# Kernel optimization log

Hardware: AMD Instinct MI355X
Metric: run time of the kernel (lower is better)

The kernel has to match this reference:

```python
import jax, jax.numpy as jnp
import numpy as np

# ---- static configuration (mirrors module init kwargs) ----
RADIUS = 8.0
MAX_NEIGHBORS = 32          # max_num_neighbors_threshold
MAX_REP = (2, 2, 0)         # static: rep = min(ceil(radius*inv_min_dist), threshold) = 2 for a1,a2; pbc[2]=False -> 0
B, N_ATOMS = 32, 128
CELL_EDGE = 4.0


def _unit_cells():
    # torch.cartesian_prod over arange(-rep, rep+1) per dim; pbc z disabled -> single 0
    ax = [np.arange(-r, r + 1, dtype=np.float32) for r in MAX_REP]
    g = np.stack(np.meshgrid(*ax, indexing='ij'), axis=-1).reshape(-1, 3)
    return jnp.asarray(g)  # [C, 3], C = 5*5*1 = 25


def setup_inputs() -> dict:
    key = jax.random.key(0)
    k1, k2 = jax.random.split(key)
    # near-cubic cells ~4A with small perturbation (keeps rep clamped at threshold=2)
    cell = (CELL_EDGE * jnp.eye(3, dtype=jnp.float32)[None] +
            0.05 * jax.random.normal(k2, (B, 3, 3), dtype=jnp.float32))
    # atoms at fractional coords in [0,1): pos = frac @ cell
    frac = jax.random.uniform(k1, (B, N_ATOMS, 3), dtype=jnp.float32)
    pos = jnp.einsum('bnf,bfk->bnk', frac, cell)
    return {'pos': pos, 'cell': cell}


def reference(pos, cell):
    """PBC radius-graph construction (gen_edges_from_batch), padded form.

    Candidate edges live on a fixed grid [B, i, j, c]: i = index1 (center atom),
    j = index2 (neighbor), c = periodic image. Returns:
      edge_dist       [B,N,N,C] f32  distance (0 where edge invalid)
      edge_cell_type  [B,N,N,C] i32  linearized cell-offset id (0 where invalid)
      edge_mask       [B,N,N,C] bool edge survives radius + self + kNN truncation
      num_neighbors_image [B]   i32  per-image edge counts (clamped), as in torch
    """
    u = _unit_cells()                         # [C,3]
    C = u.shape[0]
    # pbc offsets: offset_c = u_c @ cell_b  (matches cell_offsets.bmm(cell))
    off = jnp.einsum('ci,bik->bck', u, cell)  # [B,C,3]

    # distance vectors: pos[index2] - pos[index1] + offset (get_pbc_distances convention)
    dvec = (pos[:, None, :, None, :] - pos[:, :, None, None, :]
            + off[:, None, None, :, :])       # [B,N,N,C,3]
    d2 = jnp.sum(dvec * dvec, axis=-1)        # [B,N,N,C]

    within = (d2 <= RADIUS * RADIUS) & (d2 > 1e-4)

    # --- sort-based neighbor truncation per center atom i (get_max_neighbors_mask) ---
    num_atoms = B * N_ATOMS
    rows = jnp.where(within, d2, jnp.inf).reshape(num_atoms, N_ATOMS * C)
    order = jnp.argsort(rows, axis=1)         # stable: ties keep (j,c) order as torch
    ranks = jnp.argsort(order, axis=1)        # inverse permutation = rank of each cand
    keep = (ranks < MAX_NEIGHBORS).reshape(B, N_ATOMS, N_ATOMS, C) & within

    # per-image clamped neighbor counts (segment_csr of clamped segment_coo)
    num_nb = jnp.sum(within, axis=(2, 3)).astype(jnp.int32)          # [B,N]
    num_neighbors_image = jnp.sum(jnp.minimum(num_nb, MAX_NEIGHBORS), axis=1)

    safe_d2 = jnp.where(keep, d2, 1.0)
    edge_dist = jnp.where(keep, jnp.sqrt(safe_d2), 0.0)

    # linearized cell type: (offsets + max_rep) . [nr1*nr2, nr1, 1] with nr = 2*rep+1
    nr = np.array([2 * r + 1 for r in MAX_REP])
    mults = jnp.asarray([nr[1] * nr[2], nr[1], 1], dtype=jnp.int32)  # matches torch code
    ct = jnp.sum((u.astype(jnp.int32) + jnp.asarray(MAX_REP, jnp.int32)) * mults, axis=-1)  # [C]
    edge_cell_type = jnp.where(keep, ct[None, None, None, :], 0).astype(jnp.int32)

    return edge_dist, edge_cell_type, keep, num_neighbors_image
```

## Files before the change

### kernel.cpp

```cpp
#include <hip/hip_runtime.h>
#include <math.h>
#include <stdint.h>

#define NATOMS   128
#define NCELLS   25
#define NCAND    (NATOMS * NCELLS)
#define MAXNB    32
#define R2       64.0f
#define BLK      256
#define KEYCAP   192
#define DCUT     6.25f

__device__ __forceinline__ float d2_exact(float4 p, float4 ctr, float4 o) {
    float dx = __fadd_rn(__fsub_rn(p.x, ctr.x), o.x);
    float dy = __fadd_rn(__fsub_rn(p.y, ctr.y), o.y);
    float dz = __fadd_rn(__fsub_rn(p.z, ctr.z), o.z);
    return __fadd_rn(__fadd_rn(__fmul_rn(dx,dx), __fmul_rn(dy,dy)),
                     __fmul_rn(dz,dz));
}

__global__ __launch_bounds__(BLK) void graph_kernel(
    const float* __restrict__ pos, const float* __restrict__ cell,
    float* __restrict__ out_dist, float* __restrict__ out_ctype,
    float* __restrict__ out_mask, float* __restrict__ ws_counts)
{
    __shared__ float4 s_pos4[NATOMS];
    __shared__ float4 s_off4[NCELLS];
    __shared__ float  s_ct[NCELLS];
    __shared__ float  s_d2[NCAND];
    __shared__ unsigned long long s_keys[KEYCAP];
    __shared__ unsigned s_hist[256];
    __shared__ unsigned s_wtot[4];
    __shared__ int s_wred[4];
    __shared__ unsigned s_cnt, s_cnt2;
    __shared__ int s_tot, s_binsel, s_need;
    __shared__ unsigned long long s_K;

    const int bi   = blockIdx.x;
    const int b    = bi >> 7;
    const int i    = bi & 127;
    const int tid  = threadIdx.x;
    const int lane = tid & 63;
    const int w    = tid >> 6;

    if (tid < NATOMS) {
        const float* p = pos + (b * NATOMS + tid) * 3;
        s_pos4[tid] = make_float4(p[0], p[1], p[2], 0.0f);
    }
    if (tid >= 160 && tid < 160 + NCELLS) {
        int c = tid - 160;
        float ux = (float)(c / 5 - 2);
        float uy = (float)(c % 5 - 2);
        float ox = __fadd_rn(__fmul_rn(ux, cell[b*9+0]), __fmul_rn(uy, cell[b*9+3]));
        float oy = __fadd_rn(__fmul_rn(ux, cell[b*9+1]), __fmul_rn(uy, cell[b*9+4]));
        float oz = __fadd_rn(__fmul_rn(ux, cell[b*9+2]), __fmul_rn(uy, cell[b*9+5]));
        s_off4[c] = make_float4(ox, oy, oz, 0.0f);
        s_ct[c] = (float)(5 * (c / 5) + 5 * (c % 5));
    }
    if (tid == 0) { s_cnt = 0; s_cnt2 = 0; s_binsel = -1; s_need = 0; s_K = ~0ULL; }
    __syncthreads();

    const float4 ctr = s_pos4[i];

    int local = 0;
    for (int g = tid; g < NCAND; g += BLK) {
        int c = g >> 7;
        int j = g & 127;
        float d2 = d2_exact(s_pos4[j], ctr, s_off4[c]);
        bool within = (d2 <= R2) && (d2 > 1e-4f);
        int f = j * NCELLS + c;
        s_d2[f] = within ? d2 : __builtin_inff();
        local += within;
        bool sel = within && (d2 < DCUT);
        unsigned long long mb = __ballot(sel);
        if (mb) {
            unsigned cnt = (unsigned)__popcll(mb);
            unsigned base = 0;
            if (lane == 0) base = atomicAdd(&s_cnt, cnt);
            base = __shfl(base, 0);
            if (sel) {
                unsigned p = base + (unsigned)__popcll(mb & ((1ULL << lane) - 1ULL));
                if (p < KEYCAP)
                    s_keys[p] = ((unsigned long long)__float_as_uint(d2) << 32)
                                | (unsigned)f;
            }
        }
    }
    for (int o = 32; o; o >>= 1) local += __shfl_down(local, o);
    if (lane == 0) s_wred[w] = local;
    __syncthreads();
    if (tid == 0) {
        int tot = s_wred[0] + s_wred[1] + s_wred[2] + s_wred[3];
        s_tot = tot;
        ws_counts[bi] = (float)(tot < MAXNB ? tot : MAXNB);
    }
    __syncthreads();

    if (s_tot > MAXNB) {
        const unsigned m = s_cnt;
        if (m >= MAXNB && m <= KEYCAP) {
            for (unsigned p = tid; p < m; p += BLK) {
                unsigned long long kp = s_keys[p];
                int r = 0;
                for (unsigned q = 0; q < m; q++) r += (s_keys[q] < kp);
                if (r == MAXNB - 1) s_K = kp;
            }
        } else {
            s_hist[tid] = 0u;
            __syncthreads();
            for (int v = tid; v < NCAND / 4; v += BLK) {
                float4 dq = ((const float4*)s_d2)[v];
                #pragma unroll
                for (int e = 0; e < 4; e++) {
                    float d2 = (&dq.x)[e];
                    if (d2 < 64.5f) {
                        int bin = (int)(d2 * 4.0f);
                        if (bin > 255) bin = 255;
                        atomicAdd(&s_hist[bin], 1u);
                    }
                }
            }
            __syncthreads();
            unsigned h = s_hist[tid];
            int v = (int)h;
            #pragma unroll
            for (int off = 1; off < 64; off <<= 1) {
                int u = __shfl_up(v, off, 64);
                if (lane >= off) v += u;
            }
            if (lane == 63) s_wtot[w] = (unsigned)v;
            __syncthreads();
            unsigned pre = 0;
            for (int ww = 0; ww < w; ww++) pre += s_wtot[ww];
            unsigned ci = (unsigned)v + pre, ce = ci - h;
            if (h > 0 && ce < MAXNB && ci >= MAXNB) {
                s_binsel = tid;
                s_need   = MAXNB - (int)ce;
            }
            __syncthreads();
            const int binsel = s_binsel, need = s_need;
            for (int f = tid; f < NCAND; f += BLK) {
                float d2 = s_d2[f];
                if (d2 < 64.5f) {
                    int bin = (int)(d2 * 4.0f);
                    if (bin > 255) bin = 255;
                    if (bin == binsel) {
                        unsigned idx = atomicAdd(&s_cnt2, 1u);
                        if (idx < KEYCAP)
                            s_keys[idx] =
                                ((unsigned long long)__float_as_uint(d2) << 32)
                                | (unsigned)f;
                    }
                }
            }
            __syncthreads();
            const int m2 = (int)s_cnt2;
            if (m2 <= KEYCAP) {
                for (int p = tid; p < m2; p += BLK) {
                    unsigned long long kp = s_keys[p];
                    int r = 0;
                    for (int q = 0; q < m2; q++) r += (s_keys[q] < kp);
                    if (r == need - 1) s_K = kp;
                }
            } else {
                for (int f = tid; f < NCAND; f += BLK) {
                    float d2 = s_d2[f];
                    if (d2 >= 64.5f) continue;
                    int bin = (int)(d2 * 4.0f);
                    if (bin > 255) bin = 255;
                    if (bin != binsel) continue;
                    unsigned long long kf =
                        ((unsigned long long)__float_as_uint(d2) << 32)
                        | (unsigned)f;
                    int r = 0;
                    for (int q = 0; q < NCAND; q++) {
                        float dq = s_d2[q];
                        if (dq >= 64.5f) continue;
                        int bq = (int)(dq * 4.0f);
                        if (bq > 255) bq = 255;
                        if (bq != binsel) continue;
                        unsigned long long kq =
                            ((unsigned long long)__float_as_uint(dq) << 32)
                            | (unsigned)q;
                        r += (kq < kf);
                    }
                    if (r == need - 1) s_K = kf;
                }
            }
        }
    }
    __syncthreads();
    const unsigned long long K = s_K;

    const long long base = (long long)bi * NCAND;
    float4* o0 = (float4*)(out_dist  + base);
    float4* o1 = (float4*)(out_ctype + base);
    float4* o2 = (float4*)(out_mask  + base);
    for (int v = tid; v < NCAND / 4; v += BLK) {
        float4 dq = ((const float4*)s_d2)[v];
        int f0 = v * 4;
        int c = f0 % NCELLS;
        float4 r0, r1, r2;
        #pragma unroll
        for (int e = 0; e < 4; e++) {
            float d2 = (&dq.x)[e];
            bool within = (d2 <= R2);
            unsigned long long key =
                ((unsigned long long)__float_as_uint(d2) << 32)
                | (unsigned)(f0 + e);
            bool keep = within && (key <= K);
            (&r0.x)[e] = keep ? sqrtf(d2) : 0.0f;
            (&r1.x)[e] = keep ? s_ct[c] : 0.0f;
            (&r2.x)[e] = keep ? 1.0f : 0.0f;
            c++; if (c == NCELLS) c = 0;
        }
        o0[v] = r0; o1[v] = r1; o2[v] = r2;
    }
}

__global__ __launch_bounds__(64) void reduce_counts(
    const float* __restrict__ ws_counts, float* __restrict__ out_nb)
{
    int b = blockIdx.x;
    int t = threadIdx.x;
    float v = ws_counts[b * NATOMS + t] + ws_counts[b * NATOMS + 64 + t];
    for (int o = 32; o; o >>= 1) v += __shfl_down(v, o);
    if (t == 0) out_nb[b] = v;
}

extern "C" void kernel_launch(void* const* d_in, const int* in_sizes, int n_in,
                              void* d_out, int out_size, void* d_ws, size_t ws_size,
                              hipStream_t stream) {
    const float* pos  = (const float*)d_in[0];
    const float* cell = (const float*)d_in[1];
    float* out = (float*)d_out;
    const long long E = 32LL * NATOMS * NATOMS * NCELLS;
    float* out_dist  = out;
    float* out_ct    = out + E;
    float* out_mask  = out + 2 * E;
    float* out_nb    = out + 3 * E;
    float* ws = (float*)d_ws;

    hipLaunchKernelGGL(graph_kernel, dim3(32 * NATOMS), dim3(BLK), 0, stream,
                       pos, cell, out_dist, out_ct, out_mask, ws);
    hipLaunchKernelGGL(reduce_counts, dim3(32), dim3(64), 0, stream,
                       ws, out_nb);
}
```

Before: 165.0 us.

## Write zero output groups early and defer only near-candidate groups

The candidate loop now runs over groups of four in storage order. Any group with no candidate under the distance cut has its zero outputs written straight away, during the distance pass. Groups that contain close candidates are recorded in a shared todo list. On the fast path, only those groups are revisited after the threshold key is found. This overlaps most of the output stores with the compute and selection phases. It adds shared atomics, a ballot per element, and a correctness dependence on the todo-cap check. If the cap or any fast-path condition fails, the kernel falls back to the full rewrite path.

```diff
diff --git a/kernel.cpp b/kernel.cpp
--- a/kernel.cpp
+++ b/kernel.cpp
@@ -5,10 +5,12 @@
 #define NATOMS   128
 #define NCELLS   25
 #define NCAND    (NATOMS * NCELLS)
+#define NGRP     (NCAND / 4)
 #define MAXNB    32
 #define R2       64.0f
 #define BLK      256
 #define KEYCAP   192
+#define TODOCAP  256
 #define DCUT     6.25f
 
 __device__ __forceinline__ float d2_exact(float4 p, float4 ctr, float4 o) {
@@ -29,10 +31,11 @@
     __shared__ float  s_ct[NCELLS];
     __shared__ float  s_d2[NCAND];
     __shared__ unsigned long long s_keys[KEYCAP];
+    __shared__ unsigned short s_todo[TODOCAP];
     __shared__ unsigned s_hist[256];
     __shared__ unsigned s_wtot[4];
     __shared__ int s_wred[4];
-    __shared__ unsigned s_cnt, s_cnt2;
+    __shared__ unsigned s_cnt, s_cnt2, s_ntodo;
     __shared__ int s_tot, s_binsel, s_need;
     __shared__ unsigned long long s_K;
 
@@ -57,37 +60,66 @@
         s_off4[c] = make_float4(ox, oy, oz, 0.0f);
         s_ct[c] = (float)(5 * (c / 5) + 5 * (c % 5));
     }
-    if (tid == 0) { s_cnt = 0; s_cnt2 = 0; s_binsel = -1; s_need = 0; s_K = ~0ULL; }
+    if (tid == 0) {
+        s_cnt = 0; s_cnt2 = 0; s_ntodo = 0;
+        s_binsel = -1; s_need = 0; s_K = ~0ULL;
+    }
     __syncthreads();
 
     const float4 ctr = s_pos4[i];
-
-    int local = 0;
-    for (int g = tid; g < NCAND; g += BLK) {
-        int c = g >> 7;
-        int j = g & 127;
-        float d2 = d2_exact(s_pos4[j], ctr, s_off4[c]);
-        bool within = (d2 <= R2) && (d2 > 1e-4f);
-        int f = j * NCELLS + c;
-        s_d2[f] = within ? d2 : __builtin_inff();
-        local += within;
-        bool sel = within && (d2 < DCUT);
-        unsigned long long mb = __ballot(sel);
-        if (mb) {
-            unsigned cnt = (unsigned)__popcll(mb);
-            unsigned base = 0;
-            if (lane == 0) base = atomicAdd(&s_cnt, cnt);
-            base = __shfl(base, 0);
-            if (sel) {
-                unsigned p = base + (unsigned)__popcll(mb & ((1ULL << lane) - 1ULL));
-                if (p < KEYCAP)
-                    s_keys[p] = ((unsigned long long)__float_as_uint(d2) << 32)
-                                | (unsigned)f;
-            }
-        }
-    }
-    for (int o = 32; o; o >>= 1) local += __shfl_down(local, o);
-    if (lane == 0) s_wred[w] = local;
+    const long long base = (long long)bi * NGRP;
+    float4* o0 = (float4*)out_dist  + base;
+    float4* o1 = (float4*)out_ctype + base;
+    float4* o2 = (float4*)out_mask  + base;
+    const float4 z4 = make_float4(0.f, 0.f, 0.f, 0.f);
+
+    int nwithin = 0;
+    #pragma unroll 1
+    for (int k = 0; k < 4; k++) {
+        int g = tid + k * BLK;
+        if (g >= NGRP) continue;
+        int f0 = g * 4;
+        int j = f0 / 25;
+        int c = f0 - j * 25;
+        float d2e[4];
+        bool cl[4];
+        bool anyclose = false;
+        #pragma unroll
+        for (int e = 0; e < 4; e++) {
+            float d2 = d2_exact(s_pos4[j], ctr, s_off4[c]);
+            bool within = (d2 <= R2) && (d2 > 1e-4f);
+            d2e[e] = within ? d2 : __builtin_inff();
+            nwithin += within;
+            cl[e] = within && (d2 < DCUT);
+            anyclose |= cl[e];
+            c++; if (c == 25) { c = 0; j++; }
+        }
+        ((float4*)s_d2)[g] = make_float4(d2e[0], d2e[1], d2e[2], d2e[3]);
+        #pragma unroll
+        for (int e = 0; e < 4; e++) {
+            unsigned long long mb = __ballot(cl[e]);
+            if (mb) {
+                unsigned cnt = (unsigned)__popcll(mb);
+                unsigned kb = 0;
+                if (lane == 0) kb = atomicAdd(&s_cnt, cnt);
+                kb = __shfl(kb, 0);
+                if (cl[e]) {
+                    unsigned p = kb + (unsigned)__popcll(mb & ((1ULL << lane) - 1ULL));
+                    if (p < KEYCAP)
+                        s_keys[p] = ((unsigned long long)__float_as_uint(d2e[e]) << 32)
+                                    | (unsigned)(f0 + e);
+                }
+            }
+        }
+        if (anyclose) {
+            unsigned u = atomicAdd(&s_ntodo, 1u);
+            if (u < TODOCAP) s_todo[u] = (unsigned short)g;
+        } else {
+            o0[g] = z4; o1[g] = z4; o2[g] = z4;
+        }
+    }
+    for (int o = 32; o; o >>= 1) nwithin += __shfl_down(nwithin, o);
+    if (lane == 0) s_wred[w] = nwithin;
     __syncthreads();
     if (tid == 0) {
         int tot = s_wred[0] + s_wred[1] + s_wred[2] + s_wred[3];
@@ -96,19 +128,46 @@
     }
     __syncthreads();
 
-    if (s_tot > MAXNB) {
-        const unsigned m = s_cnt;
-        if (m >= MAXNB && m <= KEYCAP) {
-            for (unsigned p = tid; p < m; p += BLK) {
-                unsigned long long kp = s_keys[p];
-                int r = 0;
-                for (unsigned q = 0; q < m; q++) r += (s_keys[q] < kp);
-                if (r == MAXNB - 1) s_K = kp;
-            }
-        } else {
+    const unsigned m = s_cnt;
+    const bool fast = (s_tot > MAXNB) && (m >= MAXNB) && (m <= KEYCAP)
+                      && (s_ntodo <= TODOCAP);
+
+    if (fast) {
+        for (unsigned p = tid; p < m; p += BLK) {
+            unsigned long long kp = s_keys[p];
+            int r = 0;
+            for (unsigned q = 0; q < m; q++) r += (s_keys[q] < kp);
+            if (r == MAXNB - 1) s_K = kp;
+        }
+        __syncthreads();
+        const unsigned long long K = s_K;
+        const int nt = (int)s_ntodo;
+        for (int u = tid; u < nt; u += BLK) {
+            int g = s_todo[u];
+            int f0 = g * 4;
+            float4 dq = ((const float4*)s_d2)[g];
+            int c = f0 % NCELLS;
+            float4 r0, r1, r2;
+            #pragma unroll
+            for (int e = 0; e < 4; e++) {
+                float d2 = (&dq.x)[e];
+                bool within = (d2 <= R2);
+                unsigned long long key =
+                    ((unsigned long long)__float_as_uint(d2) << 32)
+                    | (unsigned)(f0 + e);
+                bool keep = within && (key <= K);
+                (&r0.x)[e] = keep ? sqrtf(d2) : 0.0f;
+                (&r1.x)[e] = keep ? s_ct[c] : 0.0f;
+                (&r2.x)[e] = keep ? 1.0f : 0.0f;
+                c++; if (c == NCELLS) c = 0;
+            }
+            o0[g] = r0; o1[g] = r1; o2[g] = r2;
+        }
+    } else {
+        if (s_tot > MAXNB) {
             s_hist[tid] = 0u;
             __syncthreads();
-            for (int v = tid; v < NCAND / 4; v += BLK) {
+            for (int v = tid; v < NGRP; v += BLK) {
                 float4 dq = ((const float4*)s_d2)[v];
                 #pragma unroll
                 for (int e = 0; e < 4; e++) {
@@ -188,33 +247,28 @@
                 }
             }
         }
-    }
-    __syncthreads();
-    const unsigned long long K = s_K;
-
-    const long long base = (long long)bi * NCAND;
-    float4* o0 = (float4*)(out_dist  + base);
-    float4* o1 = (float4*)(out_ctype + base);
-    float4* o2 = (float4*)(out_mask  + base);
-    for (int v = tid; v < NCAND / 4; v += BLK) {
-        float4 dq = ((const float4*)s_d2)[v];
-        int f0 = v * 4;
-        int c = f0 % NCELLS;
-        float4 r0, r1, r2;
-        #pragma unroll
-        for (int e = 0; e < 4; e++) {
-            float d2 = (&dq.x)[e];
-            bool within = (d2 <= R2);
-            unsigned long long key =
-                ((unsigned long long)__float_as_uint(d2) << 32)
-                | (unsigned)(f0 + e);
-            bool keep = within && (key <= K);
-            (&r0.x)[e] = keep ? sqrtf(d2) : 0.0f;
-            (&r1.x)[e] = keep ? s_ct[c] : 0.0f;
-            (&r2.x)[e] = keep ? 1.0f : 0.0f;
-            c++; if (c == NCELLS) c = 0;
-        }
-        o0[v] = r0; o1[v] = r1; o2[v] = r2;
+        __syncthreads();
+        const unsigned long long K = s_K;
+        for (int v = tid; v < NGRP; v += BLK) {
+            float4 dq = ((const float4*)s_d2)[v];
+            int f0 = v * 4;
+            int c = f0 % NCELLS;
+            float4 r0, r1, r2;
+            #pragma unroll
+            for (int e = 0; e < 4; e++) {
+                float d2 = (&dq.x)[e];
+                bool within = (d2 <= R2);
+                unsigned long long key =
+                    ((unsigned long long)__float_as_uint(d2) << 32)
+                    | (unsigned)(f0 + e);
+                bool keep = within && (key <= K);
+                (&r0.x)[e] = keep ? sqrtf(d2) : 0.0f;
+                (&r1.x)[e] = keep ? s_ct[c] : 0.0f;
+                (&r2.x)[e] = keep ? 1.0f : 0.0f;
+                c++; if (c == NCELLS) c = 0;
+            }
+            o0[v] = r0; o1[v] = r1; o2[v] = r2;
+        }
     }
 }
 
```

New measurement: 191.3 us. 1.16x slower.

## Split threshold selection into a wave-per-atom kernel ahead of the streaming write kernel

Applied to the files above, without the earlier changes.

A new select kernel has one wavefront per center atom compute distances, count neighbours and find the 32nd-smallest key with a wave-local ballot compaction and rank search, storing the threshold to workspace. The write kernel then recomputes distances on the fly and streams the three outputs without staging distances in shared memory or synchronising for selection, except for a histogram fallback path. The count reduction is folded into the write kernel, so there are still two launches. The cost is computing distances twice and an extra round trip through workspace, in exchange for a lean, bandwidth-bound write pass.

```diff
diff --git a/kernel.cpp b/kernel.cpp
--- a/kernel.cpp
+++ b/kernel.cpp
@@ -10,6 +10,8 @@
 #define BLK      256
 #define KEYCAP   192
 #define DCUT     6.25f
+#define ALLPASS  ((((unsigned long long)0x7F800000u) << 32) | 0xFFFFFFFFull)
+#define FALLBK   (~0ULL)
 
 __device__ __forceinline__ float d2_exact(float4 p, float4 ctr, float4 o) {
     float dx = __fadd_rn(__fsub_rn(p.x, ctr.x), o.x);
@@ -19,10 +21,96 @@
                      __fmul_rn(dz,dz));
 }
 
-__global__ __launch_bounds__(BLK) void graph_kernel(
+__global__ __launch_bounds__(BLK) void select_kernel(
     const float* __restrict__ pos, const float* __restrict__ cell,
+    unsigned long long* __restrict__ ws_K, float* __restrict__ ws_counts)
+{
+    __shared__ float4 s_pos4[NATOMS];
+    __shared__ float4 s_off4[NCELLS];
+    __shared__ unsigned long long s_wkeys[4][KEYCAP];
+
+    const int blk  = blockIdx.x;
+    const int b    = blk >> 5;
+    const int tid  = threadIdx.x;
+    const int lane = tid & 63;
+    const int wave = tid >> 6;
+    const int bi   = (blk << 2) + wave;
+    const int i    = bi & 127;
+
+    if (tid < NATOMS) {
+        const float* p = pos + (b * NATOMS + tid) * 3;
+        s_pos4[tid] = make_float4(p[0], p[1], p[2], 0.0f);
+    }
+    if (tid >= 160 && tid < 160 + NCELLS) {
+        int c = tid - 160;
+        float ux = (float)(c / 5 - 2);
+        float uy = (float)(c % 5 - 2);
+        float ox = __fadd_rn(__fmul_rn(ux, cell[b*9+0]), __fmul_rn(uy, cell[b*9+3]));
+        float oy = __fadd_rn(__fmul_rn(ux, cell[b*9+1]), __fmul_rn(uy, cell[b*9+4]));
+        float oz = __fadd_rn(__fmul_rn(ux, cell[b*9+2]), __fmul_rn(uy, cell[b*9+5]));
+        s_off4[c] = make_float4(ox, oy, oz, 0.0f);
+    }
+    __syncthreads();
+
+    const float4 ctr = s_pos4[i];
+    const unsigned long long lmlt = (1ULL << lane) - 1ULL;
+
+    unsigned base = 0;
+    int tot = 0;
+    #pragma unroll 1
+    for (int k = 0; k < 50; k++) {
+        int g = lane + (k << 6);
+        int c = g >> 7;
+        int j = g & 127;
+        float d2 = d2_exact(s_pos4[j], ctr, s_off4[c]);
+        bool within = (d2 <= R2) && (d2 > 1e-4f);
+        tot += within;
+        bool sel = within && (d2 < DCUT);
+        unsigned long long mb = __ballot(sel);
+        if (sel) {
+            unsigned p = base + (unsigned)__popcll(mb & lmlt);
+            if (p < KEYCAP)
+                s_wkeys[wave][p] =
+                    ((unsigned long long)__float_as_uint(d2) << 32)
+                    | (unsigned)(j * NCELLS + c);
+        }
+        base += (unsigned)__popcll(mb);
+    }
+    for (int o = 32; o; o >>= 1) tot += __shfl_down(tot, o);
+    const int tot_all = __shfl(tot, 0);
+    const int m = (int)base;
+
+    unsigned long long K;
+    if (tot_all <= MAXNB) {
+        K = ALLPASS;
+    } else if (m >= MAXNB && m <= KEYCAP) {
+        unsigned long long kl = ~0ULL;
+        for (int p = lane; p < m; p += 64) {
+            unsigned long long kp = s_wkeys[wave][p];
+            int r = 0;
+            for (int q = 0; q < m; q++) r += (s_wkeys[wave][q] < kp);
+            if (r == MAXNB - 1) kl = kp;
+        }
+        for (int o = 32; o; o >>= 1) {
+            unsigned long long other = __shfl_down(kl, o);
+            if (other < kl) kl = other;
+        }
+        K = __shfl(kl, 0);
+    } else {
+        K = FALLBK;
+    }
+    if (lane == 0) {
+        ws_K[bi] = K;
+        ws_counts[bi] = (float)(tot_all < MAXNB ? tot_all : MAXNB);
+    }
+}
+
+__global__ __launch_bounds__(BLK) void write_kernel(
+    const float* __restrict__ pos, const float* __restrict__ cell,
+    const unsigned long long* __restrict__ ws_K,
+    const float* __restrict__ ws_counts,
     float* __restrict__ out_dist, float* __restrict__ out_ctype,
-    float* __restrict__ out_mask, float* __restrict__ ws_counts)
+    float* __restrict__ out_mask, float* __restrict__ out_nb)
 {
     __shared__ float4 s_pos4[NATOMS];
     __shared__ float4 s_off4[NCELLS];
@@ -31,10 +119,9 @@
     __shared__ unsigned long long s_keys[KEYCAP];
     __shared__ unsigned s_hist[256];
     __shared__ unsigned s_wtot[4];
-    __shared__ int s_wred[4];
-    __shared__ unsigned s_cnt, s_cnt2;
-    __shared__ int s_tot, s_binsel, s_need;
-    __shared__ unsigned long long s_K;
+    __shared__ unsigned s_cnt2;
+    __shared__ int s_binsel, s_need;
+    __shared__ unsigned long long s_Ksh;
 
     const int bi   = blockIdx.x;
     const int b    = bi >> 7;
@@ -57,175 +144,156 @@
         s_off4[c] = make_float4(ox, oy, oz, 0.0f);
         s_ct[c] = (float)(5 * (c / 5) + 5 * (c % 5));
     }
-    if (tid == 0) { s_cnt = 0; s_cnt2 = 0; s_binsel = -1; s_need = 0; s_K = ~0ULL; }
+    if (tid == 0) { s_cnt2 = 0; s_binsel = -1; s_need = 0; s_Ksh = ~0ULL; }
     __syncthreads();
 
     const float4 ctr = s_pos4[i];
 
-    int local = 0;
-    for (int g = tid; g < NCAND; g += BLK) {
-        int c = g >> 7;
-        int j = g & 127;
-        float d2 = d2_exact(s_pos4[j], ctr, s_off4[c]);
-        bool within = (d2 <= R2) && (d2 > 1e-4f);
-        int f = j * NCELLS + c;
-        s_d2[f] = within ? d2 : __builtin_inff();
-        local += within;
-        bool sel = within && (d2 < DCUT);
-        unsigned long long mb = __ballot(sel);
-        if (mb) {
-            unsigned cnt = (unsigned)__popcll(mb);
-            unsigned base = 0;
-            if (lane == 0) base = atomicAdd(&s_cnt, cnt);
-            base = __shfl(base, 0);
-            if (sel) {
-                unsigned p = base + (unsigned)__popcll(mb & ((1ULL << lane) - 1ULL));
-                if (p < KEYCAP)
-                    s_keys[p] = ((unsigned long long)__float_as_uint(d2) << 32)
-                                | (unsigned)f;
-            }
-        }
-    }
-    for (int o = 32; o; o >>= 1) local += __shfl_down(local, o);
-    if (lane == 0) s_wred[w] = local;
-    __syncthreads();
-    if (tid == 0) {
-        int tot = s_wred[0] + s_wred[1] + s_wred[2] + s_wred[3];
-        s_tot = tot;
-        ws_counts[bi] = (float)(tot < MAXNB ? tot : MAXNB);
-    }
-    __syncthreads();
-
-    if (s_tot > MAXNB) {
-        const unsigned m = s_cnt;
-        if (m >= MAXNB && m <= KEYCAP) {
-            for (unsigned p = tid; p < m; p += BLK) {
-                unsigned long long kp = s_keys[p];
-                int r = 0;
-                for (unsigned q = 0; q < m; q++) r += (s_keys[q] < kp);
-                if (r == MAXNB - 1) s_K = kp;
-            }
-        } else {
-            s_hist[tid] = 0u;
-            __syncthreads();
-            for (int v = tid; v < NCAND / 4; v += BLK) {
-                float4 dq = ((const float4*)s_d2)[v];
-                #pragma unroll
-                for (int e = 0; e < 4; e++) {
-                    float d2 = (&dq.x)[e];
-                    if (d2 < 64.5f) {
-                        int bin = (int)(d2 * 4.0f);
-                        if (bin > 255) bin = 255;
-                        atomicAdd(&s_hist[bin], 1u);
-                    }
-                }
-            }
-            __syncthreads();
-            unsigned h = s_hist[tid];
-            int v = (int)h;
+    if (i == 0 && tid < 64) {
+        float v = ws_counts[(b << 7) + tid] + ws_counts[(b << 7) + 64 + tid];
+        for (int o = 32; o; o >>= 1) v += __shfl_down(v, o);
+        if (tid == 0) out_nb[b] = v;
+    }
+
+    unsigned long long K = ws_K[bi];
+
+    const long long base = (long long)bi * (NCAND / 4);
+    float4* o0 = (float4*)out_dist  + base;
+    float4* o1 = (float4*)out_ctype + base;
+    float4* o2 = (float4*)out_mask  + base;
+
+    if ((unsigned)(K >> 32) != 0xFFFFFFFFu) {
+        for (int v = tid; v < NCAND / 4; v += BLK) {
+            int f0 = v * 4;
+            int j = f0 / 25;
+            int c = f0 - j * 25;
+            float4 r0, r1, r2;
             #pragma unroll
-            for (int off = 1; off < 64; off <<= 1) {
-                int u = __shfl_up(v, off, 64);
-                if (lane >= off) v += u;
-            }
-            if (lane == 63) s_wtot[w] = (unsigned)v;
-            __syncthreads();
-            unsigned pre = 0;
-            for (int ww = 0; ww < w; ww++) pre += s_wtot[ww];
-            unsigned ci = (unsigned)v + pre, ce = ci - h;
-            if (h > 0 && ce < MAXNB && ci >= MAXNB) {
-                s_binsel = tid;
-                s_need   = MAXNB - (int)ce;
-            }
-            __syncthreads();
-            const int binsel = s_binsel, need = s_need;
-            for (int f = tid; f < NCAND; f += BLK) {
-                float d2 = s_d2[f];
+            for (int e = 0; e < 4; e++) {
+                float d2 = d2_exact(s_pos4[j], ctr, s_off4[c]);
+                bool within = (d2 <= R2) && (d2 > 1e-4f);
+                unsigned long long key =
+                    ((unsigned long long)__float_as_uint(d2) << 32)
+                    | (unsigned)(f0 + e);
+                bool keep = within && (key <= K);
+                (&r0.x)[e] = keep ? sqrtf(d2) : 0.0f;
+                (&r1.x)[e] = keep ? s_ct[c] : 0.0f;
+                (&r2.x)[e] = keep ? 1.0f : 0.0f;
+                c++; if (c == NCELLS) { c = 0; j++; }
+            }
+            o0[v] = r0; o1[v] = r1; o2[v] = r2;
+        }
+    } else {
+        for (int g = tid; g < NCAND; g += BLK) {
+            int c = g >> 7, j = g & 127;
+            float d2 = d2_exact(s_pos4[j], ctr, s_off4[c]);
+            bool within = (d2 <= R2) && (d2 > 1e-4f);
+            s_d2[j * NCELLS + c] = within ? d2 : __builtin_inff();
+        }
+        s_hist[tid] = 0u;
+        __syncthreads();
+        for (int v = tid; v < NCAND / 4; v += BLK) {
+            float4 dq = ((const float4*)s_d2)[v];
+            #pragma unroll
+            for (int e = 0; e < 4; e++) {
+                float d2 = (&dq.x)[e];
                 if (d2 < 64.5f) {
                     int bin = (int)(d2 * 4.0f);
                     if (bin > 255) bin = 255;
-                    if (bin == binsel) {
-                        unsigned idx = atomicAdd(&s_cnt2, 1u);
-                        if (idx < KEYCAP)
-                            s_keys[idx] =
-                                ((unsigned long long)__float_as_uint(d2) << 32)
-                                | (unsigned)f;
-                    }
+                    atomicAdd(&s_hist[bin], 1u);
                 }
             }
-            __syncthreads();
-            const int m2 = (int)s_cnt2;
-            if (m2 <= KEYCAP) {
-                for (int p = tid; p < m2; p += BLK) {
-                    unsigned long long kp = s_keys[p];
-                    int r = 0;
-                    for (int q = 0; q < m2; q++) r += (s_keys[q] < kp);
-                    if (r == need - 1) s_K = kp;
+        }
+        __syncthreads();
+        unsigned h = s_hist[tid];
+        int v = (int)h;
+        #pragma unroll
+        for (int off = 1; off < 64; off <<= 1) {
+            int u = __shfl_up(v, off, 64);
+            if (lane >= off) v += u;
+        }
+        if (lane == 63) s_wtot[w] = (unsigned)v;
+        __syncthreads();
+        unsigned pre = 0;
+        for (int ww = 0; ww < w; ww++) pre += s_wtot[ww];
+        unsigned ci = (unsigned)v + pre, ce = ci - h;
+        if (h > 0 && ce < MAXNB && ci >= MAXNB) {
+            s_binsel = tid;
+            s_need   = MAXNB - (int)ce;
+        }
+        __syncthreads();
+        const int binsel = s_binsel, need = s_need;
+        for (int f = tid; f < NCAND; f += BLK) {
+            float d2 = s_d2[f];
+            if (d2 < 64.5f) {
+                int bin = (int)(d2 * 4.0f);
+                if (bin > 255) bin = 255;
+                if (bin == binsel) {
+                    unsigned idx = atomicAdd(&s_cnt2, 1u);
+                    if (idx < KEYCAP)
+                        s_keys[idx] =
+                            ((unsigned long long)__float_as_uint(d2) << 32)
+                            | (unsigned)f;
                 }
-            } else {
-                for (int f = tid; f < NCAND; f += BLK) {
-                    float d2 = s_d2[f];
-                    if (d2 >= 64.5f) continue;
-                    int bin = (int)(d2 * 4.0f);
-                    if (bin > 255) bin = 255;
-                    if (bin != binsel) continue;
-                    unsigned long long kf =
-                        ((unsigned long long)__float_as_uint(d2) << 32)
-                        | (unsigned)f;
-                    int r = 0;
-                    for (int q = 0; q < NCAND; q++) {
-                        float dq = s_d2[q];
-                        if (dq >= 64.5f) continue;
-                        int bq = (int)(dq * 4.0f);
-                        if (bq > 255) bq = 255;
-                        if (bq != binsel) continue;
-                        unsigned long long kq =
-                            ((unsigned long long)__float_as_uint(dq) << 32)
-                            | (unsigned)q;
-                        r += (kq < kf);
-                    }
-                    if (r == need - 1) s_K = kf;
+            }
+        }
+        __syncthreads();
+        const int m2 = (int)s_cnt2;
+        if (m2 <= KEYCAP) {
+            for (int p = tid; p < m2; p += BLK) {
+                unsigned long long kp = s_keys[p];
+                int r = 0;
+                for (int q = 0; q < m2; q++) r += (s_keys[q] < kp);
+                if (r == need - 1) s_Ksh = kp;
+            }
+        } else {
+            for (int f = tid; f < NCAND; f += BLK) {
+                float d2 = s_d2[f];
+                if (d2 >= 64.5f) continue;
+                int bin = (int)(d2 * 4.0f);
+                if (bin > 255) bin = 255;
+                if (bin != binsel) continue;
+                unsigned long long kf =
+                    ((unsigned long long)__float_as_uint(d2) << 32)
+                    | (unsigned)f;
+                int r = 0;
+                for (int q = 0; q < NCAND; q++) {
+                    float dq = s_d2[q];
+                    if (dq >= 64.5f) continue;
+                    int bq = (int)(dq * 4.0f);
+                    if (bq > 255) bq = 255;
+                    if (bq != binsel) continue;
+                    unsigned long long kq =
+                        ((unsigned long long)__float_as_uint(dq) << 32)
+                        | (unsigned)q;
+                    r += (kq < kf);
                 }
-            }
-        }
-    }
-    __syncthreads();
-    const unsigned long long K = s_K;
-
-    const long long base = (long long)bi * NCAND;
-    float4* o0 = (float4*)(out_dist  + base);
-    float4* o1 = (float4*)(out_ctype + base);
-    float4* o2 = (float4*)(out_mask  + base);
-    for (int v = tid; v < NCAND / 4; v += BLK) {
-        float4 dq = ((const float4*)s_d2)[v];
-        int f0 = v * 4;
-        int c = f0 % NCELLS;
-        float4 r0, r1, r2;
-        #pragma unroll
-        for (int e = 0; e < 4; e++) {
-            float d2 = (&dq.x)[e];
-            bool within = (d2 <= R2);
-            unsigned long long key =
-                ((unsigned long long)__float_as_uint(d2) << 32)
-                | (unsigned)(f0 + e);
-            bool keep = within && (key <= K);
-            (&r0.x)[e] = keep ? sqrtf(d2) : 0.0f;
-            (&r1.x)[e] = keep ? s_ct[c] : 0.0f;
-            (&r2.x)[e] = keep ? 1.0f : 0.0f;
-            c++; if (c == NCELLS) c = 0;
-        }
-        o0[v] = r0; o1[v] = r1; o2[v] = r2;
-    }
-}
-
-__global__ __launch_bounds__(64) void reduce_counts(
-    const float* __restrict__ ws_counts, float* __restrict__ out_nb)
-{
-    int b = blockIdx.x;
-    int t = threadIdx.x;
-    float v = ws_counts[b * NATOMS + t] + ws_counts[b * NATOMS + 64 + t];
-    for (int o = 32; o; o >>= 1) v += __shfl_down(v, o);
-    if (t == 0) out_nb[b] = v;
+                if (r == need - 1) s_Ksh = kf;
+            }
+        }
+        __syncthreads();
+        K = s_Ksh;
+        for (int v2 = tid; v2 < NCAND / 4; v2 += BLK) {
+            float4 dq = ((const float4*)s_d2)[v2];
+            int f0 = v2 * 4;
+            int c = f0 % NCELLS;
+            float4 r0, r1, r2;
+            #pragma unroll
+            for (int e = 0; e < 4; e++) {
+                float d2 = (&dq.x)[e];
+                bool within = (d2 <= R2);
+                unsigned long long key =
+                    ((unsigned long long)__float_as_uint(d2) << 32)
+                    | (unsigned)(f0 + e);
+                bool keep = within && (key <= K);
+                (&r0.x)[e] = keep ? sqrtf(d2) : 0.0f;
+                (&r1.x)[e] = keep ? s_ct[c] : 0.0f;
+                (&r2.x)[e] = keep ? 1.0f : 0.0f;
+                c++; if (c == NCELLS) c = 0;
+            }
+            o0[v2] = r0; o1[v2] = r1; o2[v2] = r2;
+        }
+    }
 }
 
 extern "C" void kernel_launch(void* const* d_in, const int* in_sizes, int n_in,
@@ -239,10 +307,13 @@
     float* out_ct    = out + E;
     float* out_mask  = out + 2 * E;
     float* out_nb    = out + 3 * E;
-    float* ws = (float*)d_ws;
-
-    hipLaunchKernelGGL(graph_kernel, dim3(32 * NATOMS), dim3(BLK), 0, stream,
-                       pos, cell, out_dist, out_ct, out_mask, ws);
-    hipLaunchKernelGGL(reduce_counts, dim3(32), dim3(64), 0, stream,
-                       ws, out_nb);
+
+    unsigned long long* ws_K = (unsigned long long*)d_ws;
+    float* ws_counts = (float*)((char*)d_ws + 32768);
+
+    hipLaunchKernelGGL(select_kernel, dim3(1024), dim3(BLK), 0, stream,
+                       pos, cell, ws_K, ws_counts);
+    hipLaunchKernelGGL(write_kernel, dim3(32 * NATOMS), dim3(BLK), 0, stream,
+                       pos, cell, ws_K, ws_counts,
+                       out_dist, out_ct, out_mask, out_nb);
 }
```

Measured after the change: 178.0 us. 7.9% more time.
